# Performance work log

Measured on AMD Instinct MI355X. Metric: run time of the kernel, lower is better.

The kernel has to match this reference:

```python
import jax, jax.numpy as jnp
import numpy as np

TAU = 0.01          # gumbel_softmax temperature
EPS = 1e-7          # tf.keras.backend.epsilon()
DEPTH = 5
N_NODES = 2 ** DEPTH - 1   # 31 internal nodes
N_LEAVES = 2 ** DEPTH      # 32 leaves


def _build_route():
    # route[l, node + dir*N_NODES] = 1 along the root-to-leaf path of leaf l
    # (same structure old_route_to_new_route produces for a perfect tree)
    route = np.zeros((N_LEAVES, 2 * N_NODES), dtype=np.float32)
    for l in range(N_LEAVES):
        node = 0
        for d in range(DEPTH):
            bit = (l >> (DEPTH - 1 - d)) & 1  # 0 = left, 1 = right
            route[l, node + bit * N_NODES] = 1.0
            node = 2 * node + 1 + bit
    return route


def setup_inputs() -> dict:
    B, F, T = 32768, 128, 100
    key = jax.random.key(0)
    k1, k2, k3, k4 = jax.random.split(key, 4)
    x = jax.random.normal(k1, (B, F), dtype=jnp.float32)
    kernel = jax.random.normal(k2, (T, F, N_NODES), dtype=jnp.float32) * 0.1
    bias = jax.random.normal(k3, (T, N_NODES), dtype=jnp.float32) * 0.1
    leaf = jax.random.normal(k4, (T, N_LEAVES), dtype=jnp.float32)
    route = jnp.asarray(_build_route())  # [L, 2N], shared tree topology
    return {"x": x, "kernel": kernel, "bias": bias, "leaf": leaf, "route": route}


def reference(x, kernel, bias, leaf, route):
    # NodeLayer: matmul(x, concat([K, -K], 1)) + concat([b, -b], 0)
    h = jnp.einsum("bf,tfn->btn", x, kernel) + bias          # [B, T, N]
    h2 = jnp.concatenate([h, -h], axis=-1)                   # [B, T, 2N]
    # activation1: log(clip(sigmoid(clip(h/tau, -32, 32)), eps, 1))
    a1 = jnp.log(jnp.clip(jax.nn.sigmoid(jnp.clip(h2 / TAU, -32.0, 32.0)), EPS, 1.0))
    # route aggregation: sum log-probs along each root->leaf path
    r = jnp.einsum("btm,lm->btl", a1, route)                 # [B, T, L]
    # activation2: exp(clip(., -32, 0)) -> leaf routing probabilities
    probs = jnp.exp(jnp.clip(r, -32.0, 0.0))
    # weight leaf values by route probabilities, sum over leaves and trees
    return jnp.einsum("btl,tl->b", probs, leaf)              # [B] raw GBM output
```

## Files before the change

kernel.cpp:

```cpp
#include <hip/hip_runtime.h>

typedef _Float16 f16x8  __attribute__((ext_vector_type(8)));
typedef float    f32x16 __attribute__((ext_vector_type(16)));
typedef float    f32x4  __attribute__((ext_vector_type(4)));

#define NTREES  100
#define WAVES   8
#define NCH     13
#define BM      32
#define KS      9
#define TSTRIDE (KS * 512)
#define SCALE   144.269504088896f

__device__ __forceinline__ int node_of_row(int sr, float& sg) {
  const int h   = (sr >> 2) & 1;
  const int reg = (sr & 3) + ((sr >> 3) << 2);
  sg = 1.0f;
  if (reg == 0) { if (h) sg = -1.0f; return 0; }
  if (reg == 1) return 1 + h;
  if (reg < 4)  return 1 + 2 * h + reg;
  if (reg < 8)  return 3 + 4 * h + reg;
  return 7 + 8 * h + reg;
}

__device__ __forceinline__ float exp2_fast(float v) {
#if __has_builtin(__builtin_amdgcn_exp2f)
  return __builtin_amdgcn_exp2f(v);
#else
  return exp2f(v);
#endif
}

__device__ __forceinline__ void sig2(float z, float& sl, float& sr) {
  float e = exp2_fast(-z);
  sl = __builtin_amdgcn_rcpf(1.0f + e);
  sr = 1.0f - sl;
}

__global__ void prep_b(const float* __restrict__ kern, const float* __restrict__ bias,
                       unsigned short* __restrict__ bws) {
  __shared__ float kt[128][32];
  __shared__ float bs[32];
  const int t = blockIdx.x, tid = threadIdx.x;
  const float* src = kern + (size_t)t * (128 * 31);
  for (int i = tid; i < 128 * 32; i += 256) {
    const int f = i >> 5, sr_ = i & 31;
    float sg; const int g = node_of_row(sr_, sg);
    kt[f][sr_] = src[f * 31 + g] * (SCALE * sg);
  }
  if (tid < 32) {
    float sg; const int g = node_of_row(tid, sg);
    bs[tid] = bias[t * 31 + g] * (SCALE * sg);
  }
  __syncthreads();
  unsigned short* dst = bws + (size_t)t * TSTRIDE;
  for (int s = tid; s < KS * 64; s += 256) {
    const int ks = s >> 6, lane = s & 63;
    const int row = lane & 31;
    const int k0 = ks * 16 + ((lane >> 5) << 3);
    f16x8 o;
    if (ks < 8) {
      #pragma unroll
      for (int j = 0; j < 8; ++j) o[j] = (_Float16)kt[k0 + j][row];
    } else {
      #pragma unroll
      for (int j = 0; j < 8; ++j) o[j] = (_Float16)0.0f;
      if (lane < 32) o[0] = (_Float16)bs[row];
    }
    *(f16x8*)(dst + s * 8) = o;
  }
}

__global__ __launch_bounds__(512, 4) void gbm_main(
    const float* __restrict__ x,
    const unsigned short* __restrict__ bws,
    const float* __restrict__ leaf,
    float* __restrict__ out)
{
  __shared__ __align__(16) unsigned char lds[KS * 64 * 16];
  float* red = (float*)lds;

  const int tid  = threadIdx.x;
  const int lane = tid & 63;
  const int w    = tid >> 6;
  const int rowbase = blockIdx.x * BM;

  for (int s = tid; s < KS * 64; s += 512) {
    const int ks = s >> 6, l = s & 63;
    f16x8 h8;
    if (ks < 8) {
      const int xrow = l & 31;
      const int k0 = ks * 16 + ((l >> 5) << 3);
      const float* px = x + (size_t)(rowbase + xrow) * 128 + k0;
      float4 v0 = *(const float4*)px;
      float4 v1 = *(const float4*)(px + 4);
      h8[0] = (_Float16)v0.x; h8[1] = (_Float16)v0.y;
      h8[2] = (_Float16)v0.z; h8[3] = (_Float16)v0.w;
      h8[4] = (_Float16)v1.x; h8[5] = (_Float16)v1.y;
      h8[6] = (_Float16)v1.z; h8[7] = (_Float16)v1.w;
    } else {
      #pragma unroll
      for (int j = 0; j < 8; ++j) h8[j] = (_Float16)0.0f;
      if (l < 32) h8[0] = (_Float16)1.0f;
    }
    *(f16x8*)(lds + s * 16) = h8;
  }

  f16x8 br[KS];
  {
    const unsigned short* bt = bws + (size_t)w * TSTRIDE;
    #pragma unroll
    for (int i = 0; i < KS; ++i)
      br[i] = *(const f16x8*)(bt + (size_t)i * 512 + lane * 8);
  }

  __syncthreads();

  const int h = lane >> 5;
  float outAcc = 0.0f;

  for (int c = 0; c < NCH; ++c) {
    const int tree = c * WAVES + w;
    const bool act = tree < NTREES;

    f32x16 acc = {};
    if (act) {
      __builtin_amdgcn_s_setprio(1);
      #pragma unroll
      for (int ks = 0; ks < KS; ++ks) {
        f16x8 bx = *(const f16x8*)(lds + (ks * 64 + lane) * 16);
        acc = __builtin_amdgcn_mfma_f32_32x32x16_f16(br[ks], bx, acc, 0, 0, 0);
      }
      __builtin_amdgcn_s_setprio(0);
    }

    if ((c + 1) * WAVES + w < NTREES) {
      const unsigned short* nb = bws + (size_t)((c + 1) * WAVES + w) * TSTRIDE;
      #pragma unroll
      for (int i = 0; i < KS; ++i)
        br[i] = *(const f16x8*)(nb + (size_t)i * 512 + lane * 8);
    }

    if (act) {
      const float* lp = leaf + (size_t)tree * 32 + (h << 4);
      f32x4 L0 = *(const f32x4*)lp;
      f32x4 L1 = *(const f32x4*)(lp + 4);
      f32x4 L2 = *(const f32x4*)(lp + 8);
      f32x4 L3 = *(const f32x4*)(lp + 12);

      float sl, sr;
      sig2(acc[0], sl, sr); const float c0 = sl;
      sig2(acc[1], sl, sr); const float a0 = c0 * sl, a1 = c0 * sr;
      sig2(acc[2], sl, sr); const float b0 = a0 * sl, b1 = a0 * sr;
      sig2(acc[3], sl, sr); const float b2 = a1 * sl, b3 = a1 * sr;
      float cum[8];
      sig2(acc[4], sl, sr); cum[0] = b0 * sl; cum[1] = b0 * sr;
      sig2(acc[5], sl, sr); cum[2] = b1 * sl; cum[3] = b1 * sr;
      sig2(acc[6], sl, sr); cum[4] = b2 * sl; cum[5] = b2 * sr;
      sig2(acc[7], sl, sr); cum[6] = b3 * sl; cum[7] = b3 * sr;

      float s = 0.0f;
      sig2(acc[8],  sl, sr); s = fmaf(cum[0], fmaf(sl, L0[0], sr * L0[1]), s);
      sig2(acc[9],  sl, sr); s = fmaf(cum[1], fmaf(sl, L0[2], sr * L0[3]), s);
      sig2(acc[10], sl, sr); s = fmaf(cum[2], fmaf(sl, L1[0], sr * L1[1]), s);
      sig2(acc[11], sl, sr); s = fmaf(cum[3], fmaf(sl, L1[2], sr * L1[3]), s);
      sig2(acc[12], sl, sr); s = fmaf(cum[4], fmaf(sl, L2[0], sr * L2[1]), s);
      sig2(acc[13], sl, sr); s = fmaf(cum[5], fmaf(sl, L2[2], sr * L2[3]), s);
      sig2(acc[14], sl, sr); s = fmaf(cum[6], fmaf(sl, L3[0], sr * L3[1]), s);
      sig2(acc[15], sl, sr); s = fmaf(cum[7], fmaf(sl, L3[2], sr * L3[3]), s);
      outAcc += s;
    }
  }

  __syncthreads();
  red[tid] = outAcc;
  __syncthreads();
  if (tid < 32) {
    float s = 0.0f;
    #pragma unroll
    for (int j = 0; j < 16; ++j)
      s += red[j * 32 + tid];
    out[rowbase + tid] = s;
  }
}

extern "C" void kernel_launch(void* const* d_in, const int* in_sizes, int n_in,
                              void* d_out, int out_size, void* d_ws, size_t ws_size,
                              hipStream_t stream) {
  const float* x    = (const float*)d_in[0];
  const float* kern = (const float*)d_in[1];
  const float* bias = (const float*)d_in[2];
  const float* leaf = (const float*)d_in[3];

  unsigned short* bws = (unsigned short*)d_ws;

  prep_b<<<NTREES, 256, 0, stream>>>(kern, bias, bws);
  gbm_main<<<32768 / BM, 512, 0, stream>>>(x, bws, leaf, (float*)d_out);
}
```

Before: 60.65 us.

## Process two 32-row tiles per block to reuse tree weights across MFMAs

Doubles the rows per block to 64 and runs two independent MFMA accumulator chains per tree, so each weight fragment held in registers is used twice per load. The scale is negated at prep time so the negation in the exponent disappears, and each leaf pair becomes a single fma via sl*(L0-L1)+L1. This halves the grid size and adds register pressure from a second accumulator set, which could hurt occupancy at launch bounds of 512x4.

```diff
diff --git a/kernel.cpp b/kernel.cpp
--- a/kernel.cpp
+++ b/kernel.cpp
@@ -7,10 +7,10 @@
 #define NTREES  100
 #define WAVES   8
 #define NCH     13
-#define BM      32
+#define BM      64
 #define KS      9
 #define TSTRIDE (KS * 512)
-#define SCALE   144.269504088896f
+#define NSCALE  (-144.269504088896f)
 
 __device__ __forceinline__ int node_of_row(int sr, float& sg) {
   const int h   = (sr >> 2) & 1;
@@ -31,10 +31,9 @@
 #endif
 }
 
-__device__ __forceinline__ void sig2(float z, float& sl, float& sr) {
-  float e = exp2_fast(-z);
-  sl = __builtin_amdgcn_rcpf(1.0f + e);
-  sr = 1.0f - sl;
+__device__ __forceinline__ float sigl(float zn) {
+  float e = exp2_fast(zn);
+  return __builtin_amdgcn_rcpf(1.0f + e);
 }
 
 __global__ void prep_b(const float* __restrict__ kern, const float* __restrict__ bias,
@@ -46,11 +45,11 @@
   for (int i = tid; i < 128 * 32; i += 256) {
     const int f = i >> 5, sr_ = i & 31;
     float sg; const int g = node_of_row(sr_, sg);
-    kt[f][sr_] = src[f * 31 + g] * (SCALE * sg);
+    kt[f][sr_] = src[f * 31 + g] * (NSCALE * sg);
   }
   if (tid < 32) {
     float sg; const int g = node_of_row(tid, sg);
-    bs[tid] = bias[t * 31 + g] * (SCALE * sg);
+    bs[tid] = bias[t * 31 + g] * (NSCALE * sg);
   }
   __syncthreads();
   unsigned short* dst = bws + (size_t)t * TSTRIDE;
@@ -71,13 +70,41 @@
   }
 }
 
+__device__ __forceinline__ float half_eval(const f32x16& a, const f32x4& L0,
+                                           const f32x4& L1, const f32x4& L2,
+                                           const f32x4& L3) {
+  float sl, sr;
+  const float c0 = sigl(a[0]);
+  sl = sigl(a[1]); sr = 1.0f - sl;
+  const float a0 = c0 * sl, a1 = c0 * sr;
+  sl = sigl(a[2]); sr = 1.0f - sl;
+  const float b0 = a0 * sl, b1 = a0 * sr;
+  sl = sigl(a[3]); sr = 1.0f - sl;
+  const float b2 = a1 * sl, b3 = a1 * sr;
+  float cum[8];
+  sl = sigl(a[4]); sr = 1.0f - sl; cum[0] = b0 * sl; cum[1] = b0 * sr;
+  sl = sigl(a[5]); sr = 1.0f - sl; cum[2] = b1 * sl; cum[3] = b1 * sr;
+  sl = sigl(a[6]); sr = 1.0f - sl; cum[4] = b2 * sl; cum[5] = b2 * sr;
+  sl = sigl(a[7]); sr = 1.0f - sl; cum[6] = b3 * sl; cum[7] = b3 * sr;
+  float s = 0.0f;
+  s = fmaf(cum[0], fmaf(sigl(a[8]),  L0[0] - L0[1], L0[1]), s);
+  s = fmaf(cum[1], fmaf(sigl(a[9]),  L0[2] - L0[3], L0[3]), s);
+  s = fmaf(cum[2], fmaf(sigl(a[10]), L1[0] - L1[1], L1[1]), s);
+  s = fmaf(cum[3], fmaf(sigl(a[11]), L1[2] - L1[3], L1[3]), s);
+  s = fmaf(cum[4], fmaf(sigl(a[12]), L2[0] - L2[1], L2[1]), s);
+  s = fmaf(cum[5], fmaf(sigl(a[13]), L2[2] - L2[3], L2[3]), s);
+  s = fmaf(cum[6], fmaf(sigl(a[14]), L3[0] - L3[1], L3[1]), s);
+  s = fmaf(cum[7], fmaf(sigl(a[15]), L3[2] - L3[3], L3[3]), s);
+  return s;
+}
+
 __global__ __launch_bounds__(512, 4) void gbm_main(
     const float* __restrict__ x,
     const unsigned short* __restrict__ bws,
     const float* __restrict__ leaf,
     float* __restrict__ out)
 {
-  __shared__ __align__(16) unsigned char lds[KS * 64 * 16];
+  __shared__ __align__(16) unsigned char lds[2 * KS * 64 * 16];
   float* red = (float*)lds;
 
   const int tid  = threadIdx.x;
@@ -85,26 +112,28 @@
   const int w    = tid >> 6;
   const int rowbase = blockIdx.x * BM;
 
-  for (int s = tid; s < KS * 64; s += 512) {
-    const int ks = s >> 6, l = s & 63;
-    f16x8 h8;
-    if (ks < 8) {
-      const int xrow = l & 31;
-      const int k0 = ks * 16 + ((l >> 5) << 3);
-      const float* px = x + (size_t)(rowbase + xrow) * 128 + k0;
-      float4 v0 = *(const float4*)px;
-      float4 v1 = *(const float4*)(px + 4);
-      h8[0] = (_Float16)v0.x; h8[1] = (_Float16)v0.y;
-      h8[2] = (_Float16)v0.z; h8[3] = (_Float16)v0.w;
-      h8[4] = (_Float16)v1.x; h8[5] = (_Float16)v1.y;
-      h8[6] = (_Float16)v1.z; h8[7] = (_Float16)v1.w;
-    } else {
-      #pragma unroll
-      for (int j = 0; j < 8; ++j) h8[j] = (_Float16)0.0f;
-      if (l < 32) h8[0] = (_Float16)1.0f;
-    }
-    *(f16x8*)(lds + s * 16) = h8;
-  }
+  #pragma unroll
+  for (int T = 0; T < 2; ++T)
+    for (int s = tid; s < KS * 64; s += 512) {
+      const int ks = s >> 6, l = s & 63;
+      f16x8 h8;
+      if (ks < 8) {
+        const int xrow = (l & 31) + T * 32;
+        const int k0 = ks * 16 + ((l >> 5) << 3);
+        const float* px = x + (size_t)(rowbase + xrow) * 128 + k0;
+        float4 v0 = *(const float4*)px;
+        float4 v1 = *(const float4*)(px + 4);
+        h8[0] = (_Float16)v0.x; h8[1] = (_Float16)v0.y;
+        h8[2] = (_Float16)v0.z; h8[3] = (_Float16)v0.w;
+        h8[4] = (_Float16)v1.x; h8[5] = (_Float16)v1.y;
+        h8[6] = (_Float16)v1.z; h8[7] = (_Float16)v1.w;
+      } else {
+        #pragma unroll
+        for (int j = 0; j < 8; ++j) h8[j] = (_Float16)0.0f;
+        if (l < 32) h8[0] = (_Float16)1.0f;
+      }
+      *(f16x8*)(lds + T * (KS * 64 * 16) + s * 16) = h8;
+    }
 
   f16x8 br[KS];
   {
@@ -117,19 +146,21 @@
   __syncthreads();
 
   const int h = lane >> 5;
-  float outAcc = 0.0f;
+  float outAcc0 = 0.0f, outAcc1 = 0.0f;
 
   for (int c = 0; c < NCH; ++c) {
     const int tree = c * WAVES + w;
     const bool act = tree < NTREES;
 
-    f32x16 acc = {};
+    f32x16 acc0 = {}, acc1 = {};
     if (act) {
       __builtin_amdgcn_s_setprio(1);
       #pragma unroll
       for (int ks = 0; ks < KS; ++ks) {
-        f16x8 bx = *(const f16x8*)(lds + (ks * 64 + lane) * 16);
-        acc = __builtin_amdgcn_mfma_f32_32x32x16_f16(br[ks], bx, acc, 0, 0, 0);
+        f16x8 bx0 = *(const f16x8*)(lds + (ks * 64 + lane) * 16);
+        f16x8 bx1 = *(const f16x8*)(lds + KS * 64 * 16 + (ks * 64 + lane) * 16);
+        acc0 = __builtin_amdgcn_mfma_f32_32x32x16_f16(br[ks], bx0, acc0, 0, 0, 0);
+        acc1 = __builtin_amdgcn_mfma_f32_32x32x16_f16(br[ks], bx1, acc1, 0, 0, 0);
       }
       __builtin_amdgcn_s_setprio(0);
     }
@@ -148,38 +179,21 @@
       f32x4 L2 = *(const f32x4*)(lp + 8);
       f32x4 L3 = *(const f32x4*)(lp + 12);
 
-      float sl, sr;
-      sig2(acc[0], sl, sr); const float c0 = sl;
-      sig2(acc[1], sl, sr); const float a0 = c0 * sl, a1 = c0 * sr;
-      sig2(acc[2], sl, sr); const float b0 = a0 * sl, b1 = a0 * sr;
-      sig2(acc[3], sl, sr); const float b2 = a1 * sl, b3 = a1 * sr;
-      float cum[8];
-      sig2(acc[4], sl, sr); cum[0] = b0 * sl; cum[1] = b0 * sr;
-      sig2(acc[5], sl, sr); cum[2] = b1 * sl; cum[3] = b1 * sr;
-      sig2(acc[6], sl, sr); cum[4] = b2 * sl; cum[5] = b2 * sr;
-      sig2(acc[7], sl, sr); cum[6] = b3 * sl; cum[7] = b3 * sr;
-
-      float s = 0.0f;
-      sig2(acc[8],  sl, sr); s = fmaf(cum[0], fmaf(sl, L0[0], sr * L0[1]), s);
-      sig2(acc[9],  sl, sr); s = fmaf(cum[1], fmaf(sl, L0[2], sr * L0[3]), s);
-      sig2(acc[10], sl, sr); s = fmaf(cum[2], fmaf(sl, L1[0], sr * L1[1]), s);
-      sig2(acc[11], sl, sr); s = fmaf(cum[3], fmaf(sl, L1[2], sr * L1[3]), s);
-      sig2(acc[12], sl, sr); s = fmaf(cum[4], fmaf(sl, L2[0], sr * L2[1]), s);
-      sig2(acc[13], sl, sr); s = fmaf(cum[5], fmaf(sl, L2[2], sr * L2[3]), s);
-      sig2(acc[14], sl, sr); s = fmaf(cum[6], fmaf(sl, L3[0], sr * L3[1]), s);
-      sig2(acc[15], sl, sr); s = fmaf(cum[7], fmaf(sl, L3[2], sr * L3[3]), s);
-      outAcc += s;
-    }
-  }
-
-  __syncthreads();
-  red[tid] = outAcc;
-  __syncthreads();
-  if (tid < 32) {
+      outAcc0 += half_eval(acc0, L0, L1, L2, L3);
+      outAcc1 += half_eval(acc1, L0, L1, L2, L3);
+    }
+  }
+
+  __syncthreads();
+  red[tid] = outAcc0;
+  red[512 + tid] = outAcc1;
+  __syncthreads();
+  if (tid < BM) {
+    const int tile = tid >> 5, r = tid & 31;
     float s = 0.0f;
     #pragma unroll
     for (int j = 0; j < 16; ++j)
-      s += red[j * 32 + tid];
+      s += red[tile * 512 + j * 32 + r];
     out[rowbase + tid] = s;
   }
 }
```

New measurement: 52.35 us. -13.7%, faster.
